# Kernel optimization log

Measured on AMD Instinct MI355X. Metric: run time of the kernel, lower is better.

## Reference

```python
import jax, jax.numpy as jnp
import numpy as np

N_KNN = 16
BN_EPS = 1e-5


def conv1d(x, w, b):
    # x: [B, Cin, N], w: [Cout, Cin], b: [Cout] (1x1 Conv1d)
    return jnp.einsum('oc,bcn->bon', w, x) + b[None, :, None]


def conv2d(x, w, b):
    # x: [B, Cin, N, K], w: [Cout, Cin], b: [Cout] (1x1 Conv2d)
    return jnp.einsum('oc,bcnk->bonk', w, x) + b[None, :, None, None]


def bn2d(x, gamma, beta, mean, var):
    # eval-mode BatchNorm2d over channel axis 1
    scale = (gamma / jnp.sqrt(var + BN_EPS))[None, :, None, None]
    return (x - mean[None, :, None, None]) * scale + beta[None, :, None, None]


def knn_idx(pos, k):
    # pos: [B, 3, N] -> idx: [B, N, K] of k nearest neighbors (incl. self)
    p = jnp.swapaxes(pos, 1, 2)  # [B, N, 3]
    sq = jnp.sum(p * p, axis=-1)  # [B, N]
    d2 = sq[:, :, None] - 2.0 * jnp.einsum('bnd,bmd->bnm', p, p) + sq[:, None, :]
    _, idx = jax.lax.top_k(-d2, k)
    return idx


def group(x, idx):
    # x: [B, C, N], idx: [B, N, K] -> [B, C, N, K] (grouping_operation)
    return jax.vmap(lambda xb, ib: xb[:, ib])(x, idx)


def setup_inputs() -> dict:
    key = jax.random.key(0)
    B, C_OBJ, C_Q, N, DIM, PH, AM = 4, 512, 512, 4096, 128, 64, 4
    ks = jax.random.split(key, 32)
    r = lambda i, sh, s=0.05: jax.random.normal(ks[i], sh, jnp.float32) * s
    inp = {
        'obj_feature': jax.random.normal(ks[0], (B, C_OBJ, N), jnp.float32),
        'pos': jax.random.normal(ks[1], (B, 3, N), jnp.float32),
        'query_points': jax.random.normal(ks[2], (B, C_Q, N), jnp.float32),
        # linear_start_query / linear_start_obj
        'w_sq': r(3, (DIM, C_Q)), 'b_sq': r(4, (DIM,)),
        'w_so': r(5, (DIM, C_OBJ)), 'b_so': r(6, (DIM,)),
        # key / query / value 1x1 convs
        'w_k': r(7, (DIM, DIM)), 'b_k': r(8, (DIM,)),
        'w_q': r(9, (DIM, DIM)), 'b_q': r(10, (DIM,)),
        'w_v': r(11, (DIM, DIM)), 'b_v': r(12, (DIM,)),
        # pos_mlp: Conv2d(3->PH), BN, ReLU, Conv2d(PH->DIM)
        'w_p1': r(13, (PH, 3)), 'b_p1': r(14, (PH,)),
        'g_bn1': 1.0 + r(15, (PH,)), 'be_bn1': r(16, (PH,)),
        'm_bn1': r(17, (PH,)), 'v_bn1': 1.0 + 0.1 * jax.random.uniform(ks[18], (PH,), jnp.float32),
        'w_p2': r(19, (DIM, PH)), 'b_p2': r(20, (DIM,)),
        # attn_mlp: Conv2d(DIM->DIM*AM), BN, ReLU, Conv2d(DIM*AM->DIM)
        'w_a1': r(21, (DIM * AM, DIM)), 'b_a1': r(22, (DIM * AM,)),
        'g_bn2': 1.0 + r(23, (DIM * AM,)), 'be_bn2': r(24, (DIM * AM,)),
        'm_bn2': r(25, (DIM * AM,)), 'v_bn2': 1.0 + 0.1 * jax.random.uniform(ks[26], (DIM * AM,), jnp.float32),
        # linear_end
        'w_e': r(27, (C_OBJ, DIM)), 'b_e': r(28, (C_OBJ,)),
    }
    return inp


def reference(obj_feature, pos, query_points, w_sq, b_sq, w_so, b_so, w_k, b_k,
              w_q, b_q, w_v, b_v, w_p1, b_p1, g_bn1, be_bn1, m_bn1, v_bn1,
              w_p2, b_p2, w_a1, b_a1, g_bn2, be_bn2, m_bn2, v_bn2, w_e, b_e):
    qf = conv1d(query_points, w_sq, b_sq)          # [B, dim, N]
    f = conv1d(obj_feature, w_so, b_so)            # [B, dim, N]
    idx = knn_idx(jax.lax.stop_gradient(pos), N_KNN)  # [B, N, K]
    key_g = group(conv1d(f, w_k, b_k), idx)        # [B, dim, N, K]
    value = conv1d(f, w_v, b_v)                    # [B, dim, N]
    query = conv1d(qf, w_q, b_q)                   # [B, dim, N]
    qk_rel = query[:, :, :, None] - key_g          # [B, dim, N, K]
    pos_rel = pos[:, :, :, None] - group(pos, idx)  # [B, 3, N, K]
    pe = conv2d(jax.nn.relu(bn2d(conv2d(pos_rel, w_p1, b_p1), g_bn1, be_bn1, m_bn1, v_bn1)), w_p2, b_p2)
    attn = conv2d(jax.nn.relu(bn2d(conv2d(qk_rel + pe, w_a1, b_a1), g_bn2, be_bn2, m_bn2, v_bn2)), w_a2_placeholder := w_p2 * 0 + 0, b_p2 * 0) if False else None
    hidden = jax.nn.relu(bn2d(conv2d(qk_rel + pe, w_a1, b_a1), g_bn2, be_bn2, m_bn2, v_bn2))
    attn = jax.nn.softmax(conv2d(hidden, w_a2, b_a2), axis=-1)  # softmax over K
    v = value[:, :, :, None] + pe                  # [B, dim, N, K]
    agg = jnp.sum(attn * v, axis=-1)               # 'b c i j, b c i j -> b c i'
    return conv1d(agg, w_e, b_e)                   # [B, C_obj, N]

# fix: w_a2/b_a2 are parameters; re-declare reference cleanly to include them

def _setup_extra(inp):
    kk = jax.random.split(jax.random.key(7), 2)
    inp['w_a2'] = jax.random.normal(kk[0], (128, 512), jnp.float32) * 0.05
    inp['b_a2'] = jax.random.normal(kk[1], (128,), jnp.float32) * 0.05
    return inp

_orig_setup = setup_inputs

def setup_inputs():
    return _setup_extra(_orig_setup())


def reference(obj_feature, pos, query_points, w_sq, b_sq, w_so, b_so, w_k, b_k,
              w_q, b_q, w_v, b_v, w_p1, b_p1, g_bn1, be_bn1, m_bn1, v_bn1,
              w_p2, b_p2, w_a1, b_a1, g_bn2, be_bn2, m_bn2, v_bn2, w_a2, b_a2,
              w_e, b_e):
    qf = conv1d(query_points, w_sq, b_sq)
    f = conv1d(obj_feature, w_so, b_so)
    idx = knn_idx(jax.lax.stop_gradient(pos), N_KNN)
    key_g = group(conv1d(f, w_k, b_k), idx)
    value = conv1d(f, w_v, b_v)
    query = conv1d(qf, w_q, b_q)
    qk_rel = query[:, :, :, None] - key_g
    pos_rel = pos[:, :, :, None] - group(pos, idx)
    pe = conv2d(jax.nn.relu(bn2d(conv2d(pos_rel, w_p1, b_p1), g_bn1, be_bn1, m_bn1, v_bn1)), w_p2, b_p2)
    hidden = jax.nn.relu(bn2d(conv2d(qk_rel + pe, w_a1, b_a1), g_bn2, be_bn2, m_bn2, v_bn2))
    attn = jax.nn.softmax(conv2d(hidden, w_a2, b_a2), axis=-1)
    v = value[:, :, :, None] + pe
    agg = jnp.sum(attn * v, axis=-1)
    return conv1d(agg, w_e, b_e)
```

## Files before the change

### kernel.cpp

```cpp
#include <hip/hip_runtime.h>

typedef __bf16 bf16;
typedef __bf16 bf16x8 __attribute__((ext_vector_type(8)));
typedef __bf16 bf16x4 __attribute__((ext_vector_type(4)));
typedef __bf16 bf16x2 __attribute__((ext_vector_type(2)));
typedef float f32x4 __attribute__((ext_vector_type(4)));

#define MFMA16(a,b,c) __builtin_amdgcn_mfma_f32_16x16x32_bf16((a),(b),(c),0,0,0)

#define NPTS 4096
#define CIN 512
#define DIM 128
#define PH 64
#define HID 512

#define OFF_WQS 0u
#define OFF_WKO (128u*1024u)
#define OFF_WVO (256u*1024u)
#define OFF_BQS (384u*1024u)
#define OFF_BKO (385u*1024u)
#define OFF_BVO (386u*1024u)
#define OFF_S1  (387u*1024u)
#define OFF_T1  (388u*1024u)
#define OFF_S2  (389u*1024u)
#define OFF_T2  (391u*1024u)
#define OFF_CW  (400u*1024u)
#define OFF_QT  (1u<<20)
#define OFF_KT  (OFF_QT + (4u<<20))
#define OFF_VT  (OFF_QT + (8u<<20))
#define OFF_IDX (OFF_QT + (12u<<20))
#define WS_NEED (OFF_QT + (13u<<20))

struct P {
  const float* in[31];
  char* ws;
  float* out;
  int ybase;
};

__device__ __forceinline__ void softbar() {
  asm volatile("s_waitcnt lgkmcnt(0)" ::: "memory");
  __builtin_amdgcn_s_barrier();
  __builtin_amdgcn_sched_barrier(0);
}

template<int C> __device__ __forceinline__ float rorf(float x){
  return __int_as_float(__builtin_amdgcn_mov_dpp(__float_as_int(x), 0x120|C, 0xF, 0xF, true));
}
__device__ __forceinline__ float red16max(float x){
  x=fmaxf(x,rorf<1>(x)); x=fmaxf(x,rorf<2>(x)); x=fmaxf(x,rorf<4>(x)); x=fmaxf(x,rorf<8>(x)); return x;
}
__device__ __forceinline__ float red16sum(float x){
  x+=rorf<1>(x); x+=rorf<2>(x); x+=rorf<4>(x); x+=rorf<8>(x); return x;
}
template<int C> __device__ __forceinline__ unsigned long long ror64(unsigned long long k){
  unsigned lo = (unsigned)__builtin_amdgcn_mov_dpp((int)(unsigned)k,        0x120|C, 0xF, 0xF, true);
  unsigned hi = (unsigned)__builtin_amdgcn_mov_dpp((int)(unsigned)(k>>32), 0x120|C, 0xF, 0xF, true);
  return ((unsigned long long)hi<<32)|lo;
}

__global__ __launch_bounds__(256) void k_fold(P p) {
  int tid = blockIdx.x*256 + threadIdx.x;
  char* ws = p.ws;
  if (tid < 196608) {
    int m_id = tid >> 16, o = (tid >> 9) & 127, c = tid & 511;
    const float* A  = m_id==0 ? p.in[9] : (m_id==1 ? p.in[7] : p.in[11]);
    const float* Bm = (m_id==0) ? p.in[3] : p.in[5];
    float acc = 0.f;
    #pragma unroll 8
    for (int m=0;m<128;m++) acc += A[o*128+m] * Bm[m*512+c];
    bf16* outw = (bf16*)(ws + (m_id==0?OFF_WQS: m_id==1?OFF_WKO:OFF_WVO));
    outw[o*512+c] = (bf16)acc;
  } else if (tid < 196992) {
    int t = tid - 196608; int m_id = t >> 7, o = t & 127;
    const float* A  = m_id==0 ? p.in[9] : (m_id==1 ? p.in[7] : p.in[11]);
    const float* bb = (m_id==0) ? p.in[4] : p.in[6];
    const float* bs = m_id==0 ? p.in[10] : (m_id==1 ? p.in[8] : p.in[12]);
    float acc = bs[o];
    for (int m=0;m<128;m++) acc += A[o*128+m] * bb[m];
    float* ob = (float*)(ws + (m_id==0?OFF_BQS: m_id==1?OFF_BKO:OFF_BVO));
    ob[o] = acc;
  } else if (tid < 197056) {
    int i = tid - 196992;
    float s = p.in[15][i] * rsqrtf(p.in[18][i] + 1e-5f);
    ((float*)(ws+OFF_S1))[i] = s;
    ((float*)(ws+OFF_T1))[i] = (p.in[14][i] - p.in[17][i])*s + p.in[16][i];
  } else if (tid < 197568) {
    int i = tid - 197056;
    float s = p.in[23][i] * rsqrtf(p.in[26][i] + 1e-5f);
    ((float*)(ws+OFF_S2))[i] = s;
    ((float*)(ws+OFF_T2))[i] = (p.in[22][i] - p.in[25][i])*s + p.in[24][i];
  } else if (tid < 223168) {
    int e0 = (tid - 197568) * 8;
    const float* src; int base;
    if (e0 < 8192)        { src = p.in[19]; base = 0; }
    else if (e0 < 73728)  { src = p.in[21]; base = 8192; }
    else if (e0 < 139264) { src = p.in[29]; base = 73728; }
    else                  { src = p.in[27]; base = 139264; }
    const float* sp = src + (e0 - base);
    f32x4 a = *(const f32x4*)sp, b2 = *(const f32x4*)(sp+4);
    bf16x8 o8;
    o8[0]=(bf16)a[0]; o8[1]=(bf16)a[1]; o8[2]=(bf16)a[2]; o8[3]=(bf16)a[3];
    o8[4]=(bf16)b2[0]; o8[5]=(bf16)b2[1]; o8[6]=(bf16)b2[2]; o8[7]=(bf16)b2[3];
    *(bf16x8*)((bf16*)(ws+OFF_CW) + e0) = o8;
  }
}

__global__ __launch_bounds__(256) void k_knnqkv(P p) {
  if (blockIdx.x < 768) {
    int qb = blockIdx.x;
    int mat = qb >> 8, b = (qb >> 6) & 3, n0 = (qb & 63) * 64;
    int tid = threadIdx.x, lane = tid&63, w = tid>>6;
    const float* in = (mat==0 ? p.in[2] : p.in[0]) + b*CIN*NPTS;
    const bf16* W = (const bf16*)(p.ws + (mat==0?OFF_WQS: mat==1?OFF_WKO:OFF_WVO));
    const float* bias = (const float*)(p.ws + (mat==0?OFF_BQS: mat==1?OFF_BKO:OFF_BVO));
    bf16* outT = (bf16*)(p.ws + (mat==0?OFF_QT: mat==1?OFF_KT:OFF_VT)) + (b*NPTS + n0)*DIM;
    __shared__ __align__(16) bf16 Bl[64*40];
    f32x4 acc[8] = {};
    for (int ks=0; ks<16; ks++) {
      int c0 = ks*32;
      {
        int cc = tid>>3, nn0 = (tid&7)*8;
        const float* sp = in + (c0+cc)*NPTS + n0 + nn0;
        f32x4 a = *(const f32x4*)sp, b2 = *(const f32x4*)(sp+4);
        Bl[(nn0+0)*40+cc]=(bf16)a[0];  Bl[(nn0+1)*40+cc]=(bf16)a[1];
        Bl[(nn0+2)*40+cc]=(bf16)a[2];  Bl[(nn0+3)*40+cc]=(bf16)a[3];
        Bl[(nn0+4)*40+cc]=(bf16)b2[0]; Bl[(nn0+5)*40+cc]=(bf16)b2[1];
        Bl[(nn0+6)*40+cc]=(bf16)b2[2]; Bl[(nn0+7)*40+cc]=(bf16)b2[3];
      }
      softbar();
      int ncol = w*16 + (lane&15);
      bf16x8 bfr = *(const bf16x8*)(&Bl[ncol*40 + (lane>>4)*8]);
      #pragma unroll
      for (int ot=0;ot<8;ot++) {
        bf16x8 af = *(const bf16x8*)(W + (ot*16 + (lane&15))*CIN + c0 + (lane>>4)*8);
        acc[ot] = MFMA16(af, bfr, acc[ot]);
      }
      softbar();
    }
    int o0 = (lane>>4)*4;
    int nloc = w*16 + (lane&15);
    #pragma unroll
    for (int ot=0;ot<8;ot++) {
      f32x4 bs = *(const f32x4*)(bias + ot*16 + o0);
      bf16x4 st;
      st[0]=(bf16)(acc[ot][0]+bs[0]); st[1]=(bf16)(acc[ot][1]+bs[1]);
      st[2]=(bf16)(acc[ot][2]+bs[2]); st[3]=(bf16)(acc[ot][3]+bs[3]);
      *(bf16x4*)(outT + nloc*DIM + ot*16 + o0) = st;
    }
    return;
  }
  int lane = threadIdx.x & 63, w = threadIdx.x >> 6;
  int ig = (blockIdx.x - 768)*4 + w;
  int b = ig >> 12, n = ig & 4095;
  const float* pb = p.in[1] + b*3*NPTS;
  float qx = pb[n], qy = pb[NPTS+n], qz = pb[2*NPTS+n];
  float sqn = __fadd_rn(__fadd_rn(__fmul_rn(qx,qx), __fmul_rn(qy,qy)), __fmul_rn(qz,qz));
  unsigned u[64];
  #pragma unroll
  for (int t=0;t<64;t++) {
    int j = t*64 + lane;
    float xj=pb[j], yj=pb[NPTS+j], zj=pb[2*NPTS+j];
    float sqj = __fadd_rn(__fadd_rn(__fmul_rn(xj,xj), __fmul_rn(yj,yj)), __fmul_rn(zj,zj));
    float dot = __fadd_rn(__fadd_rn(__fmul_rn(qx,xj), __fmul_rn(qy,yj)), __fmul_rn(qz,zj));
    float d2 = __fadd_rn(__fsub_rn(sqn, __fmul_rn(2.f,dot)), sqj);
    unsigned bb2 = __float_as_uint(d2);
    u[t] = bb2 ^ (((unsigned)((int)bb2 >> 31)) | 0x80000000u);
  }
  unsigned v0=u[0], v1=u[16], v2=u[32], v3=u[48];
  int t0=0, t1=16, t2=32, t3=48;
  #pragma unroll
  for (int i=1;i<16;i++) {
    { bool lt=u[i]    <v0; v0=lt?u[i]   :v0; t0=lt?(i)   :t0; }
    { bool lt=u[16+i] <v1; v1=lt?u[16+i]:v1; t1=lt?(16+i):t1; }
    { bool lt=u[32+i] <v2; v2=lt?u[32+i]:v2; t2=lt?(32+i):t2; }
    { bool lt=u[48+i] <v3; v3=lt?u[48+i]:v3; t3=lt?(48+i):t3; }
  }
  int* op = (int*)(p.ws + OFF_IDX) + ig*16;
  #pragma unroll 1
  for (int r=0;r<16;r++) {
    unsigned va=v0; int ta=t0;
    { bool lt=v1<va; va=lt?v1:va; ta=lt?t1:ta; }
    unsigned vb=v2; int tb=t2;
    { bool lt=v3<vb; vb=lt?v3:vb; tb=lt?t3:tb; }
    { bool lt=vb<va; va=lt?vb:va; ta=lt?tb:ta; }
    unsigned long long key = ((unsigned long long)va << 12) | (unsigned)((ta<<6) | lane);
    { unsigned long long o = ror64<1>(key); if (o<key) key=o; }
    { unsigned long long o = ror64<2>(key); if (o<key) key=o; }
    { unsigned long long o = ror64<4>(key); if (o<key) key=o; }
    { unsigned long long o = ror64<8>(key); if (o<key) key=o; }
    { unsigned long long o = __shfl_xor(key,16); if (o<key) key=o; }
    { unsigned long long o = __shfl_xor(key,32); if (o<key) key=o; }
    unsigned jwin = (unsigned)key & 4095u;
    if (lane==0) op[r] = (int)jwin;
    if (r==15) break;
    int tsel = __builtin_amdgcn_readfirstlane((int)(jwin>>6));
    bool mine = ((int)(jwin&63)==lane);
    switch (tsel) {
#define CLR(T) case T: u[T] = mine ? 0xFFFFFFFFu : u[T]; break;
      CLR(0) CLR(1) CLR(2) CLR(3) CLR(4) CLR(5) CLR(6) CLR(7)
      CLR(8) CLR(9) CLR(10) CLR(11) CLR(12) CLR(13) CLR(14) CLR(15)
      CLR(16) CLR(17) CLR(18) CLR(19) CLR(20) CLR(21) CLR(22) CLR(23)
      CLR(24) CLR(25) CLR(26) CLR(27) CLR(28) CLR(29) CLR(30) CLR(31)
      CLR(32) CLR(33) CLR(34) CLR(35) CLR(36) CLR(37) CLR(38) CLR(39)
      CLR(40) CLR(41) CLR(42) CLR(43) CLR(44) CLR(45) CLR(46) CLR(47)
      CLR(48) CLR(49) CLR(50) CLR(51) CLR(52) CLR(53) CLR(54) CLR(55)
      CLR(56) CLR(57) CLR(58) CLR(59) CLR(60) CLR(61) CLR(62) CLR(63)
#undef CLR
      default: break;
    }
    switch (tsel >> 4) {
      case 0: { v0=u[0]; t0=0;
        #pragma unroll
        for (int i=1;i<16;i++){ bool lt=u[i]<v0; v0=lt?u[i]:v0; t0=lt?i:t0; } } break;
      case 1: { v1=u[16]; t1=16;
        #pragma unroll
        for (int i=1;i<16;i++){ bool lt=u[16+i]<v1; v1=lt?u[16+i]:v1; t1=lt?(16+i):t1; } } break;
      case 2: { v2=u[32]; t2=32;
        #pragma unroll
        for (int i=1;i<16;i++){ bool lt=u[32+i]<v2; v2=lt?u[32+i]:v2; t2=lt?(32+i):t2; } } break;
      default: { v3=u[48]; t3=48;
        #pragma unroll
        for (int i=1;i<16;i++){ bool lt=u[48+i]<v3; v3=lt?u[48+i]:v3; t3=lt?(48+i):t3; } } break;
    }
  }
}

__global__ __launch_bounds__(512) void k_fused(P p) {
  int bb = p.ybase + blockIdx.y, pt0 = blockIdx.x*8;
  int tid=threadIdx.x, lane=tid&63, w=tid>>6;
  int c = lane&15, g = lane>>4;
  char* ws = p.ws;
  const bf16* qT = (const bf16*)(ws+OFF_QT) + bb*NPTS*DIM;
  const bf16* kT = (const bf16*)(ws+OFF_KT) + bb*NPTS*DIM;
  const bf16* vT = (const bf16*)(ws+OFF_VT) + bb*NPTS*DIM;
  const int* idxg = (const int*)(ws+OFF_IDX) + (bb*NPTS + pt0)*16;
  const bf16* wp2b = (const bf16*)(ws+OFF_CW);
  const bf16* wa1b = wp2b + 8192;
  const bf16* wa2b = wa1b + 65536;
  const bf16* web  = wa2b + 65536;
  const float* s2 = (const float*)(ws+OFF_S2);
  const float* t2 = (const float*)(ws+OFF_T2);
  __shared__ __align__(16) char LB[53248];
  bf16* Xl = (bf16*)LB;
  bf16* HT = (bf16*)(LB + 34816);
  bf16* aggl = (bf16*)(LB + 34816);

  {
    int col = w*16 + c;
    int j = idxg[col] & 4095;
    const float* pb = p.in[1] + bb*3*NPTS;
    int n = pt0 + w;
    float r0 = pb[n]-pb[j], r1 = pb[NPTS+n]-pb[NPTS+j], r2 = pb[2*NPTS+n]-pb[2*NPTS+j];
    const float* wp1 = p.in[13];
    const float* s1 = (const float*)(ws+OFF_S1);
    const float* t1 = (const float*)(ws+OFF_T1);
    #pragma unroll
    for (int i=0;i<16;i+=2) {
      int m = g*16 + i;
      float x0 = wp1[m*3]*r0   + wp1[m*3+1]*r1 + wp1[m*3+2]*r2;
      float x1 = wp1[m*3+3]*r0 + wp1[m*3+4]*r1 + wp1[m*3+5]*r2;
      bf16x2 pk;
      pk[0] = (bf16)fmaxf(0.f, x0*s1[m]   + t1[m]);
      pk[1] = (bf16)fmaxf(0.f, x1*s1[m+1] + t1[m+1]);
      *(bf16x2*)(&HT[col*72 + m]) = pk;
    }
  }
  softbar();

  {
    f32x4 acc[8] = {};
    int crow = w*16 + c;
    #pragma unroll
    for (int ksx=0; ksx<2; ksx++) {
      int m0 = ksx*32 + g*8;
      bf16x8 af = *(const bf16x8*)(wp2b + crow*PH + m0);
      #pragma unroll
      for (int nt=0; nt<8; nt++) {
        int col = nt*16 + c;
        bf16x8 bfr = *(const bf16x8*)(&HT[col*72 + m0]);
        acc[nt] = MFMA16(af, bfr, acc[nt]);
      }
    }
    int c0 = w*16 + g*4;
    f32x4 bp4 = *(const f32x4*)(p.in[20] + c0);
    #pragma unroll
    for (int nt=0; nt<8; nt++) {
      int col = nt*16 + c;
      int j = idxg[col] & 4095;
      int n = pt0 + nt;
      bf16x4 q4 = *(const bf16x4*)(qT + n*DIM + c0);
      bf16x4 k4 = *(const bf16x4*)(kT + j*DIM + c0);
      bf16x4 st;
      #pragma unroll
      for (int r=0;r<4;r++)
        st[r] = (bf16)((float)q4[r] - (float)k4[r] + acc[nt][r] + bp4[r]);
      *(bf16x4*)(&Xl[col*136 + c0]) = st;
    }
  }
  softbar();

  f32x4 S[8] = {};
  for (int ch=0; ch<8; ch++) {
    f32x4 acc1[4] = {};
    int mtw = w & 3, nbase = (w>>2)*4;
    int hrow = ch*64 + mtw*16 + c;
    #pragma unroll
    for (int ksx=0; ksx<4; ksx++) {
      bf16x8 af = *(const bf16x8*)(wa1b + hrow*DIM + ksx*32 + g*8);
      #pragma unroll
      for (int i=0; i<4; i++) {
        int col = (nbase+i)*16 + c;
        bf16x8 bfr = *(const bf16x8*)(&Xl[col*136 + ksx*32 + g*8]);
        acc1[i] = MFMA16(af, bfr, acc1[i]);
      }
    }
    int h0 = ch*64 + mtw*16 + g*4;
    int h0loc = mtw*16 + g*4;
    f32x4 sv = *(const f32x4*)(s2 + h0);
    f32x4 tv = *(const f32x4*)(t2 + h0);
    #pragma unroll
    for (int i=0;i<4;i++) {
      int col = (nbase+i)*16 + c;
      bf16x4 st;
      st[0]=(bf16)fmaxf(0.f, acc1[i][0]*sv[0]+tv[0]);
      st[1]=(bf16)fmaxf(0.f, acc1[i][1]*sv[1]+tv[1]);
      st[2]=(bf16)fmaxf(0.f, acc1[i][2]*sv[2]+tv[2]);
      st[3]=(bf16)fmaxf(0.f, acc1[i][3]*sv[3]+tv[3]);
      *(bf16x4*)(&HT[col*72 + h0loc]) = st;
    }
    softbar();
    int orow = w*16 + c;
    #pragma unroll
    for (int ksx=0; ksx<2; ksx++) {
      bf16x8 af = *(const bf16x8*)(wa2b + orow*HID + ch*64 + ksx*32 + g*8);
      #pragma unroll
      for (int nt=0; nt<8; nt++) {
        int col = nt*16 + c;
        bf16x8 bfr = *(const bf16x8*)(&HT[col*72 + ksx*32 + g*8]);
        S[nt] = MFMA16(af, bfr, S[nt]);
      }
    }
    softbar();
  }

  {
    int c0 = w*16 + g*4;
    #pragma unroll
    for (int nt=0; nt<8; nt++) {
      f32x4 s = S[nt];
      int col = nt*16 + c;
      int j = idxg[col] & 4095;
      int n = pt0 + nt;
      bf16x4 x4 = *(const bf16x4*)(&Xl[col*136 + c0]);
      bf16x4 q4 = *(const bf16x4*)(qT + n*DIM + c0);
      bf16x4 k4 = *(const bf16x4*)(kT + j*DIM + c0);
      bf16x4 v4 = *(const bf16x4*)(vT + n*DIM + c0);
      float agv[4];
      #pragma unroll
      for (int r=0;r<4;r++) {
        float mx = red16max(s[r]);
        float e = __expf(s[r]-mx);
        float sm = red16sum(e);
        float at = e/sm;
        float vpe = (float)v4[r] + (float)x4[r] - (float)q4[r] + (float)k4[r];
        agv[r] = red16sum(at*vpe);
      }
      if (c==0) {
        bf16x4 st; st[0]=(bf16)agv[0]; st[1]=(bf16)agv[1]; st[2]=(bf16)agv[2]; st[3]=(bf16)agv[3];
        *(bf16x4*)(&aggl[nt*136 + c0]) = st;
      }
    }
  }
  softbar();

  {
    const float* be = p.in[28];
    f32x4 acc5[4] = {};
    #pragma unroll
    for (int ksx=0; ksx<4; ksx++) {
      bf16x8 bfr = *(const bf16x8*)(&aggl[c*136 + ksx*32 + g*8]);
      #pragma unroll
      for (int i=0;i<4;i++) {
        int e = (w*4+i)*16 + c;
        bf16x8 af = *(const bf16x8*)(web + e*DIM + ksx*32 + g*8);
        acc5[i] = MFMA16(af, bfr, acc5[i]);
      }
    }
    if (c < 8) {
      int n = pt0 + c;
      #pragma unroll
      for (int i=0;i<4;i++) {
        int e0 = (w*4+i)*16 + g*4;
        f32x4 be4 = *(const f32x4*)(be + e0);
        #pragma unroll
        for (int r=0;r<4;r++)
          p.out[(bb*CIN + e0+r)*NPTS + n] = acc5[i][r] + be4[r];
      }
    }
  }
}

extern "C" void kernel_launch(void* const* d_in, const int* in_sizes, int n_in,
                              void* d_out, int out_size, void* d_ws, size_t ws_size,
                              hipStream_t stream) {
  if (ws_size < WS_NEED || n_in < 31) return;
  P p;
  for (int i=0;i<31;i++) p.in[i] = (const float*)d_in[i];
  p.ws = (char*)d_ws;
  p.out = (float*)d_out;
  p.ybase = 0;
  k_fold<<<872, 256, 0, stream>>>(p);
  k_knnqkv<<<768 + 4096, 256, 0, stream>>>(p);
  k_fused<<<dim3(512, 4), 512, 0, stream>>>(p);
}
```

Before: 400.5 us.

## XOR-swizzle LDS tiles instead of padding and prefetch gathered key rows

Replaces the padded LDS layouts (row strides of 136 and 72 elements) for the X and hidden tiles with unpadded power-of-two rows and an XOR swizzle on the column index. This avoids bank conflicts while shrinking shared memory from 53248 to 49152 bytes. It also loads the kNN indices and gathered key vectors into registers once at kernel start, so they are not re-gathered from global memory in two phases. The trade-off is more live registers (the k4p and jn arrays) across the main loop, which may raise register pressure.

```diff
diff --git a/kernel.cpp b/kernel.cpp
--- a/kernel.cpp
+++ b/kernel.cpp
@@ -226,6 +226,9 @@
   }
 }
 
+#define XLB(LBp, col, off2) ((bf16*)((LBp) + (((((col)<<8) + ((off2)<<1))) ^ ((((col)&7))<<4))))
+#define HTB(LBp, col, off2) ((bf16*)((LBp) + 32768 + (((((col)<<7) + ((off2)<<1))) ^ ((((col)&7))<<4))))
+
 __global__ __launch_bounds__(512) void k_fused(P p) {
   int bb = p.ybase + blockIdx.y, pt0 = blockIdx.x*8;
   int tid=threadIdx.x, lane=tid&63, w=tid>>6;
@@ -241,14 +244,20 @@
   const bf16* web  = wa2b + 65536;
   const float* s2 = (const float*)(ws+OFF_S2);
   const float* t2 = (const float*)(ws+OFF_T2);
-  __shared__ __align__(16) char LB[53248];
-  bf16* Xl = (bf16*)LB;
-  bf16* HT = (bf16*)(LB + 34816);
-  bf16* aggl = (bf16*)(LB + 34816);
+  __shared__ __align__(16) char LB[49152];
+  bf16* aggl = (bf16*)(LB + 32768);
+
+  int c0 = w*16 + g*4;
+  int jn[8];
+  #pragma unroll
+  for (int nt=0;nt<8;nt++) jn[nt] = idxg[nt*16 + c] & 4095;
+  bf16x4 k4p[8];
+  #pragma unroll
+  for (int nt=0;nt<8;nt++) k4p[nt] = *(const bf16x4*)(kT + jn[nt]*DIM + c0);
 
   {
     int col = w*16 + c;
-    int j = idxg[col] & 4095;
+    int j = jn[w];
     const float* pb = p.in[1] + bb*3*NPTS;
     int n = pt0 + w;
     float r0 = pb[n]-pb[j], r1 = pb[NPTS+n]-pb[NPTS+j], r2 = pb[2*NPTS+n]-pb[2*NPTS+j];
@@ -263,7 +272,7 @@
       bf16x2 pk;
       pk[0] = (bf16)fmaxf(0.f, x0*s1[m]   + t1[m]);
       pk[1] = (bf16)fmaxf(0.f, x1*s1[m+1] + t1[m+1]);
-      *(bf16x2*)(&HT[col*72 + m]) = pk;
+      *(bf16x2*)HTB(LB, col, m) = pk;
     }
   }
   softbar();
@@ -278,24 +287,22 @@
       #pragma unroll
       for (int nt=0; nt<8; nt++) {
         int col = nt*16 + c;
-        bf16x8 bfr = *(const bf16x8*)(&HT[col*72 + m0]);
+        bf16x8 bfr = *(const bf16x8*)HTB(LB, col, m0);
         acc[nt] = MFMA16(af, bfr, acc[nt]);
       }
     }
-    int c0 = w*16 + g*4;
     f32x4 bp4 = *(const f32x4*)(p.in[20] + c0);
     #pragma unroll
     for (int nt=0; nt<8; nt++) {
       int col = nt*16 + c;
-      int j = idxg[col] & 4095;
       int n = pt0 + nt;
       bf16x4 q4 = *(const bf16x4*)(qT + n*DIM + c0);
-      bf16x4 k4 = *(const bf16x4*)(kT + j*DIM + c0);
+      bf16x4 k4 = k4p[nt];
       bf16x4 st;
       #pragma unroll
       for (int r=0;r<4;r++)
         st[r] = (bf16)((float)q4[r] - (float)k4[r] + acc[nt][r] + bp4[r]);
-      *(bf16x4*)(&Xl[col*136 + c0]) = st;
+      *(bf16x4*)XLB(LB, col, c0) = st;
     }
   }
   softbar();
@@ -311,7 +318,7 @@
       #pragma unroll
       for (int i=0; i<4; i++) {
         int col = (nbase+i)*16 + c;
-        bf16x8 bfr = *(const bf16x8*)(&Xl[col*136 + ksx*32 + g*8]);
+        bf16x8 bfr = *(const bf16x8*)XLB(LB, col, ksx*32 + g*8);
         acc1[i] = MFMA16(af, bfr, acc1[i]);
       }
     }
@@ -327,7 +334,7 @@
       st[1]=(bf16)fmaxf(0.f, acc1[i][1]*sv[1]+tv[1]);
       st[2]=(bf16)fmaxf(0.f, acc1[i][2]*sv[2]+tv[2]);
       st[3]=(bf16)fmaxf(0.f, acc1[i][3]*sv[3]+tv[3]);
-      *(bf16x4*)(&HT[col*72 + h0loc]) = st;
+      *(bf16x4*)HTB(LB, col, h0loc) = st;
     }
     softbar();
     int orow = w*16 + c;
@@ -337,7 +344,7 @@
       #pragma unroll
       for (int nt=0; nt<8; nt++) {
         int col = nt*16 + c;
-        bf16x8 bfr = *(const bf16x8*)(&HT[col*72 + ksx*32 + g*8]);
+        bf16x8 bfr = *(const bf16x8*)HTB(LB, col, ksx*32 + g*8);
         S[nt] = MFMA16(af, bfr, S[nt]);
       }
     }
@@ -345,16 +352,14 @@
   }
 
   {
-    int c0 = w*16 + g*4;
     #pragma unroll
     for (int nt=0; nt<8; nt++) {
       f32x4 s = S[nt];
       int col = nt*16 + c;
-      int j = idxg[col] & 4095;
       int n = pt0 + nt;
-      bf16x4 x4 = *(const bf16x4*)(&Xl[col*136 + c0]);
+      bf16x4 x4 = *(const bf16x4*)XLB(LB, col, c0);
       bf16x4 q4 = *(const bf16x4*)(qT + n*DIM + c0);
-      bf16x4 k4 = *(const bf16x4*)(kT + j*DIM + c0);
+      bf16x4 k4 = k4p[nt];
       bf16x4 v4 = *(const bf16x4*)(vT + n*DIM + c0);
       float agv[4];
       #pragma unroll
```

Result: slower. 455.1 us (+13.6%).

## Fuse KNN selection into main fused kernel, keep indices in LDS

Applied to the files above, without the earlier changes.

Moves the per-point KNN distance computation and top-16 selection out of the combined qkv/knn kernel into the start of the fused attention kernel. Each of the 8 waves computes neighbours for one point and writes them to shared memory, so the global index buffer write/read round trip goes away. The qkv kernel now launches only the projection blocks. The trade-off is that the fused kernel, launched with 512 threads per block, takes on a register-heavy 64-entry selection phase, which can raise register pressure and cut occupancy for the whole kernel. It also loses the overlap the separate KNN blocks had with the projection GEMM blocks.

```diff
diff --git a/kernel.cpp b/kernel.cpp
--- a/kernel.cpp
+++ b/kernel.cpp
@@ -106,123 +106,46 @@
   }
 }
 
-__global__ __launch_bounds__(256) void k_knnqkv(P p) {
-  if (blockIdx.x < 768) {
-    int qb = blockIdx.x;
-    int mat = qb >> 8, b = (qb >> 6) & 3, n0 = (qb & 63) * 64;
-    int tid = threadIdx.x, lane = tid&63, w = tid>>6;
-    const float* in = (mat==0 ? p.in[2] : p.in[0]) + b*CIN*NPTS;
-    const bf16* W = (const bf16*)(p.ws + (mat==0?OFF_WQS: mat==1?OFF_WKO:OFF_WVO));
-    const float* bias = (const float*)(p.ws + (mat==0?OFF_BQS: mat==1?OFF_BKO:OFF_BVO));
-    bf16* outT = (bf16*)(p.ws + (mat==0?OFF_QT: mat==1?OFF_KT:OFF_VT)) + (b*NPTS + n0)*DIM;
-    __shared__ __align__(16) bf16 Bl[64*40];
-    f32x4 acc[8] = {};
-    for (int ks=0; ks<16; ks++) {
-      int c0 = ks*32;
-      {
-        int cc = tid>>3, nn0 = (tid&7)*8;
-        const float* sp = in + (c0+cc)*NPTS + n0 + nn0;
-        f32x4 a = *(const f32x4*)sp, b2 = *(const f32x4*)(sp+4);
-        Bl[(nn0+0)*40+cc]=(bf16)a[0];  Bl[(nn0+1)*40+cc]=(bf16)a[1];
-        Bl[(nn0+2)*40+cc]=(bf16)a[2];  Bl[(nn0+3)*40+cc]=(bf16)a[3];
-        Bl[(nn0+4)*40+cc]=(bf16)b2[0]; Bl[(nn0+5)*40+cc]=(bf16)b2[1];
-        Bl[(nn0+6)*40+cc]=(bf16)b2[2]; Bl[(nn0+7)*40+cc]=(bf16)b2[3];
-      }
-      softbar();
-      int ncol = w*16 + (lane&15);
-      bf16x8 bfr = *(const bf16x8*)(&Bl[ncol*40 + (lane>>4)*8]);
-      #pragma unroll
-      for (int ot=0;ot<8;ot++) {
-        bf16x8 af = *(const bf16x8*)(W + (ot*16 + (lane&15))*CIN + c0 + (lane>>4)*8);
-        acc[ot] = MFMA16(af, bfr, acc[ot]);
-      }
-      softbar();
-    }
-    int o0 = (lane>>4)*4;
-    int nloc = w*16 + (lane&15);
+__global__ __launch_bounds__(256) void k_qkv(P p) {
+  int qb = blockIdx.x;
+  int mat = qb >> 8, b = (qb >> 6) & 3, n0 = (qb & 63) * 64;
+  int tid = threadIdx.x, lane = tid&63, w = tid>>6;
+  const float* in = (mat==0 ? p.in[2] : p.in[0]) + b*CIN*NPTS;
+  const bf16* W = (const bf16*)(p.ws + (mat==0?OFF_WQS: mat==1?OFF_WKO:OFF_WVO));
+  const float* bias = (const float*)(p.ws + (mat==0?OFF_BQS: mat==1?OFF_BKO:OFF_BVO));
+  bf16* outT = (bf16*)(p.ws + (mat==0?OFF_QT: mat==1?OFF_KT:OFF_VT)) + (b*NPTS + n0)*DIM;
+  __shared__ __align__(16) bf16 Bl[64*40];
+  f32x4 acc[8] = {};
+  for (int ks=0; ks<16; ks++) {
+    int c0 = ks*32;
+    {
+      int cc = tid>>3, nn0 = (tid&7)*8;
+      const float* sp = in + (c0+cc)*NPTS + n0 + nn0;
+      f32x4 a = *(const f32x4*)sp, b2 = *(const f32x4*)(sp+4);
+      Bl[(nn0+0)*40+cc]=(bf16)a[0];  Bl[(nn0+1)*40+cc]=(bf16)a[1];
+      Bl[(nn0+2)*40+cc]=(bf16)a[2];  Bl[(nn0+3)*40+cc]=(bf16)a[3];
+      Bl[(nn0+4)*40+cc]=(bf16)b2[0]; Bl[(nn0+5)*40+cc]=(bf16)b2[1];
+      Bl[(nn0+6)*40+cc]=(bf16)b2[2]; Bl[(nn0+7)*40+cc]=(bf16)b2[3];
+    }
+    softbar();
+    int ncol = w*16 + (lane&15);
+    bf16x8 bfr = *(const bf16x8*)(&Bl[ncol*40 + (lane>>4)*8]);
     #pragma unroll
     for (int ot=0;ot<8;ot++) {
-      f32x4 bs = *(const f32x4*)(bias + ot*16 + o0);
-      bf16x4 st;
-      st[0]=(bf16)(acc[ot][0]+bs[0]); st[1]=(bf16)(acc[ot][1]+bs[1]);
-      st[2]=(bf16)(acc[ot][2]+bs[2]); st[3]=(bf16)(acc[ot][3]+bs[3]);
-      *(bf16x4*)(outT + nloc*DIM + ot*16 + o0) = st;
-    }
-    return;
-  }
-  int lane = threadIdx.x & 63, w = threadIdx.x >> 6;
-  int ig = (blockIdx.x - 768)*4 + w;
-  int b = ig >> 12, n = ig & 4095;
-  const float* pb = p.in[1] + b*3*NPTS;
-  float qx = pb[n], qy = pb[NPTS+n], qz = pb[2*NPTS+n];
-  float sqn = __fadd_rn(__fadd_rn(__fmul_rn(qx,qx), __fmul_rn(qy,qy)), __fmul_rn(qz,qz));
-  unsigned u[64];
+      bf16x8 af = *(const bf16x8*)(W + (ot*16 + (lane&15))*CIN + c0 + (lane>>4)*8);
+      acc[ot] = MFMA16(af, bfr, acc[ot]);
+    }
+    softbar();
+  }
+  int o0 = (lane>>4)*4;
+  int nloc = w*16 + (lane&15);
   #pragma unroll
-  for (int t=0;t<64;t++) {
-    int j = t*64 + lane;
-    float xj=pb[j], yj=pb[NPTS+j], zj=pb[2*NPTS+j];
-    float sqj = __fadd_rn(__fadd_rn(__fmul_rn(xj,xj), __fmul_rn(yj,yj)), __fmul_rn(zj,zj));
-    float dot = __fadd_rn(__fadd_rn(__fmul_rn(qx,xj), __fmul_rn(qy,yj)), __fmul_rn(qz,zj));
-    float d2 = __fadd_rn(__fsub_rn(sqn, __fmul_rn(2.f,dot)), sqj);
-    unsigned bb2 = __float_as_uint(d2);
-    u[t] = bb2 ^ (((unsigned)((int)bb2 >> 31)) | 0x80000000u);
-  }
-  unsigned v0=u[0], v1=u[16], v2=u[32], v3=u[48];
-  int t0=0, t1=16, t2=32, t3=48;
-  #pragma unroll
-  for (int i=1;i<16;i++) {
-    { bool lt=u[i]    <v0; v0=lt?u[i]   :v0; t0=lt?(i)   :t0; }
-    { bool lt=u[16+i] <v1; v1=lt?u[16+i]:v1; t1=lt?(16+i):t1; }
-    { bool lt=u[32+i] <v2; v2=lt?u[32+i]:v2; t2=lt?(32+i):t2; }
-    { bool lt=u[48+i] <v3; v3=lt?u[48+i]:v3; t3=lt?(48+i):t3; }
-  }
-  int* op = (int*)(p.ws + OFF_IDX) + ig*16;
-  #pragma unroll 1
-  for (int r=0;r<16;r++) {
-    unsigned va=v0; int ta=t0;
-    { bool lt=v1<va; va=lt?v1:va; ta=lt?t1:ta; }
-    unsigned vb=v2; int tb=t2;
-    { bool lt=v3<vb; vb=lt?v3:vb; tb=lt?t3:tb; }
-    { bool lt=vb<va; va=lt?vb:va; ta=lt?tb:ta; }
-    unsigned long long key = ((unsigned long long)va << 12) | (unsigned)((ta<<6) | lane);
-    { unsigned long long o = ror64<1>(key); if (o<key) key=o; }
-    { unsigned long long o = ror64<2>(key); if (o<key) key=o; }
-    { unsigned long long o = ror64<4>(key); if (o<key) key=o; }
-    { unsigned long long o = ror64<8>(key); if (o<key) key=o; }
-    { unsigned long long o = __shfl_xor(key,16); if (o<key) key=o; }
-    { unsigned long long o = __shfl_xor(key,32); if (o<key) key=o; }
-    unsigned jwin = (unsigned)key & 4095u;
-    if (lane==0) op[r] = (int)jwin;
-    if (r==15) break;
-    int tsel = __builtin_amdgcn_readfirstlane((int)(jwin>>6));
-    bool mine = ((int)(jwin&63)==lane);
-    switch (tsel) {
-#define CLR(T) case T: u[T] = mine ? 0xFFFFFFFFu : u[T]; break;
-      CLR(0) CLR(1) CLR(2) CLR(3) CLR(4) CLR(5) CLR(6) CLR(7)
-      CLR(8) CLR(9) CLR(10) CLR(11) CLR(12) CLR(13) CLR(14) CLR(15)
-      CLR(16) CLR(17) CLR(18) CLR(19) CLR(20) CLR(21) CLR(22) CLR(23)
-      CLR(24) CLR(25) CLR(26) CLR(27) CLR(28) CLR(29) CLR(30) CLR(31)
-      CLR(32) CLR(33) CLR(34) CLR(35) CLR(36) CLR(37) CLR(38) CLR(39)
-      CLR(40) CLR(41) CLR(42) CLR(43) CLR(44) CLR(45) CLR(46) CLR(47)
-      CLR(48) CLR(49) CLR(50) CLR(51) CLR(52) CLR(53) CLR(54) CLR(55)
-      CLR(56) CLR(57) CLR(58) CLR(59) CLR(60) CLR(61) CLR(62) CLR(63)
-#undef CLR
-      default: break;
-    }
-    switch (tsel >> 4) {
-      case 0: { v0=u[0]; t0=0;
-        #pragma unroll
-        for (int i=1;i<16;i++){ bool lt=u[i]<v0; v0=lt?u[i]:v0; t0=lt?i:t0; } } break;
-      case 1: { v1=u[16]; t1=16;
-        #pragma unroll
-        for (int i=1;i<16;i++){ bool lt=u[16+i]<v1; v1=lt?u[16+i]:v1; t1=lt?(16+i):t1; } } break;
-      case 2: { v2=u[32]; t2=32;
-        #pragma unroll
-        for (int i=1;i<16;i++){ bool lt=u[32+i]<v2; v2=lt?u[32+i]:v2; t2=lt?(32+i):t2; } } break;
-      default: { v3=u[48]; t3=48;
-        #pragma unroll
-        for (int i=1;i<16;i++){ bool lt=u[48+i]<v3; v3=lt?u[48+i]:v3; t3=lt?(48+i):t3; } } break;
-    }
+  for (int ot=0;ot<8;ot++) {
+    f32x4 bs = *(const f32x4*)(bias + ot*16 + o0);
+    bf16x4 st;
+    st[0]=(bf16)(acc[ot][0]+bs[0]); st[1]=(bf16)(acc[ot][1]+bs[1]);
+    st[2]=(bf16)(acc[ot][2]+bs[2]); st[3]=(bf16)(acc[ot][3]+bs[3]);
+    *(bf16x4*)(outT + nloc*DIM + ot*16 + o0) = st;
   }
 }
 
@@ -234,7 +157,6 @@
   const bf16* qT = (const bf16*)(ws+OFF_QT) + bb*NPTS*DIM;
   const bf16* kT = (const bf16*)(ws+OFF_KT) + bb*NPTS*DIM;
   const bf16* vT = (const bf16*)(ws+OFF_VT) + bb*NPTS*DIM;
-  const int* idxg = (const int*)(ws+OFF_IDX) + (bb*NPTS + pt0)*16;
   const bf16* wp2b = (const bf16*)(ws+OFF_CW);
   const bf16* wa1b = wp2b + 8192;
   const bf16* wa2b = wa1b + 65536;
@@ -245,11 +167,87 @@
   bf16* Xl = (bf16*)LB;
   bf16* HT = (bf16*)(LB + 34816);
   bf16* aggl = (bf16*)(LB + 34816);
+  __shared__ int idxl[128];
+
+  const float* pb = p.in[1] + bb*3*NPTS;
+
+  {
+    int n = pt0 + w;
+    float qx = pb[n], qy = pb[NPTS+n], qz = pb[2*NPTS+n];
+    float sqn = __fadd_rn(__fadd_rn(__fmul_rn(qx,qx), __fmul_rn(qy,qy)), __fmul_rn(qz,qz));
+    unsigned u[64];
+    #pragma unroll
+    for (int t=0;t<64;t++) {
+      int j = t*64 + lane;
+      float xj=pb[j], yj=pb[NPTS+j], zj=pb[2*NPTS+j];
+      float sqj = __fadd_rn(__fadd_rn(__fmul_rn(xj,xj), __fmul_rn(yj,yj)), __fmul_rn(zj,zj));
+      float dot = __fadd_rn(__fadd_rn(__fmul_rn(qx,xj), __fmul_rn(qy,yj)), __fmul_rn(qz,zj));
+      float d2 = __fadd_rn(__fsub_rn(sqn, __fmul_rn(2.f,dot)), sqj);
+      unsigned bb2 = __float_as_uint(d2);
+      u[t] = bb2 ^ (((unsigned)((int)bb2 >> 31)) | 0x80000000u);
+    }
+    unsigned v0=u[0], v1=u[16], v2=u[32], v3=u[48];
+    int t0=0, t1=16, t2_=32, t3=48;
+    #pragma unroll
+    for (int i=1;i<16;i++) {
+      { bool lt=u[i]    <v0; v0=lt?u[i]   :v0; t0=lt?(i)   :t0; }
+      { bool lt=u[16+i] <v1; v1=lt?u[16+i]:v1; t1=lt?(16+i):t1; }
+      { bool lt=u[32+i] <v2; v2=lt?u[32+i]:v2; t2_=lt?(32+i):t2_; }
+      { bool lt=u[48+i] <v3; v3=lt?u[48+i]:v3; t3=lt?(48+i):t3; }
+    }
+    #pragma unroll 1
+    for (int r=0;r<16;r++) {
+      unsigned va=v0; int ta=t0;
+      { bool lt=v1<va; va=lt?v1:va; ta=lt?t1:ta; }
+      unsigned vb=v2; int tb=t2_;
+      { bool lt=v3<vb; vb=lt?v3:vb; tb=lt?t3:tb; }
+      { bool lt=vb<va; va=lt?vb:va; ta=lt?tb:ta; }
+      unsigned long long key = ((unsigned long long)va << 12) | (unsigned)((ta<<6) | lane);
+      { unsigned long long o = ror64<1>(key); if (o<key) key=o; }
+      { unsigned long long o = ror64<2>(key); if (o<key) key=o; }
+      { unsigned long long o = ror64<4>(key); if (o<key) key=o; }
+      { unsigned long long o = ror64<8>(key); if (o<key) key=o; }
+      { unsigned long long o = __shfl_xor(key,16); if (o<key) key=o; }
+      { unsigned long long o = __shfl_xor(key,32); if (o<key) key=o; }
+      unsigned jwin = (unsigned)key & 4095u;
+      if (lane==0) idxl[w*16 + r] = (int)jwin;
+      if (r==15) break;
+      int tsel = __builtin_amdgcn_readfirstlane((int)(jwin>>6));
+      bool mine = ((int)(jwin&63)==lane);
+      switch (tsel) {
+#define CLR(T) case T: u[T] = mine ? 0xFFFFFFFFu : u[T]; break;
+        CLR(0) CLR(1) CLR(2) CLR(3) CLR(4) CLR(5) CLR(6) CLR(7)
+        CLR(8) CLR(9) CLR(10) CLR(11) CLR(12) CLR(13) CLR(14) CLR(15)
+        CLR(16) CLR(17) CLR(18) CLR(19) CLR(20) CLR(21) CLR(22) CLR(23)
+        CLR(24) CLR(25) CLR(26) CLR(27) CLR(28) CLR(29) CLR(30) CLR(31)
+        CLR(32) CLR(33) CLR(34) CLR(35) CLR(36) CLR(37) CLR(38) CLR(39)
+        CLR(40) CLR(41) CLR(42) CLR(43) CLR(44) CLR(45) CLR(46) CLR(47)
+        CLR(48) CLR(49) CLR(50) CLR(51) CLR(52) CLR(53) CLR(54) CLR(55)
+        CLR(56) CLR(57) CLR(58) CLR(59) CLR(60) CLR(61) CLR(62) CLR(63)
+#undef CLR
+        default: break;
+      }
+      switch (tsel >> 4) {
+        case 0: { v0=u[0]; t0=0;
+          #pragma unroll
+          for (int i=1;i<16;i++){ bool lt=u[i]<v0; v0=lt?u[i]:v0; t0=lt?i:t0; } } break;
+        case 1: { v1=u[16]; t1=16;
+          #pragma unroll
+          for (int i=1;i<16;i++){ bool lt=u[16+i]<v1; v1=lt?u[16+i]:v1; t1=lt?(16+i):t1; } } break;
+        case 2: { v2=u[32]; t2_=32;
+          #pragma unroll
+          for (int i=1;i<16;i++){ bool lt=u[32+i]<v2; v2=lt?u[32+i]:v2; t2_=lt?(32+i):t2_; } } break;
+        default: { v3=u[48]; t3=48;
+          #pragma unroll
+          for (int i=1;i<16;i++){ bool lt=u[48+i]<v3; v3=lt?u[48+i]:v3; t3=lt?(48+i):t3; } } break;
+      }
+    }
+  }
+  softbar();
 
   {
     int col = w*16 + c;
-    int j = idxg[col] & 4095;
-    const float* pb = p.in[1] + bb*3*NPTS;
+    int j = idxl[col];
     int n = pt0 + w;
     float r0 = pb[n]-pb[j], r1 = pb[NPTS+n]-pb[NPTS+j], r2 = pb[2*NPTS+n]-pb[2*NPTS+j];
     const float* wp1 = p.in[13];
@@ -287,7 +285,7 @@
     #pragma unroll
     for (int nt=0; nt<8; nt++) {
       int col = nt*16 + c;
-      int j = idxg[col] & 4095;
+      int j = idxl[col];
       int n = pt0 + nt;
       bf16x4 q4 = *(const bf16x4*)(qT + n*DIM + c0);
       bf16x4 k4 = *(const bf16x4*)(kT + j*DIM + c0);
@@ -350,7 +348,7 @@
     for (int nt=0; nt<8; nt++) {
       f32x4 s = S[nt];
       int col = nt*16 + c;
-      int j = idxg[col] & 4095;
+      int j = idxl[col];
       int n = pt0 + nt;
       bf16x4 x4 = *(const bf16x4*)(&Xl[col*136 + c0]);
       bf16x4 q4 = *(const bf16x4*)(qT + n*DIM + c0);
@@ -411,6 +409,6 @@
   p.out = (float*)d_out;
   p.ybase = 0;
   k_fold<<<872, 256, 0, stream>>>(p);
-  k_knnqkv<<<768 + 4096, 256, 0, stream>>>(p);
+  k_qkv<<<768, 256, 0, stream>>>(p);
   k_fused<<<dim3(512, 4), 512, 0, stream>>>(p);
 }
```

Result: slower. 466.9 us (+16.6%).

## Split KNN top-k search across four waves per query with shared-memory merge

Applied to the files above, without the earlier changes.

The KNN selection now assigns one block of four waves to each query point instead of one wave per point. Each wave holds 16 candidate distances per lane rather than 64 and publishes its running minimum to shared memory, where the four slots are merged each round. Only the wave owning the winner rescans its candidates. This aims to reduce register pressure and raise occupancy and parallelism, at the cost of block barriers per extraction round and idle waves during the rescan.

```diff
diff --git a/kernel.cpp b/kernel.cpp
--- a/kernel.cpp
+++ b/kernel.cpp
@@ -107,10 +107,10 @@
 }
 
 __global__ __launch_bounds__(256) void k_knnqkv(P p) {
+  int tid = threadIdx.x, lane = tid&63, w = tid>>6;
   if (blockIdx.x < 768) {
     int qb = blockIdx.x;
     int mat = qb >> 8, b = (qb >> 6) & 3, n0 = (qb & 63) * 64;
-    int tid = threadIdx.x, lane = tid&63, w = tid>>6;
     const float* in = (mat==0 ? p.in[2] : p.in[0]) + b*CIN*NPTS;
     const bf16* W = (const bf16*)(p.ws + (mat==0?OFF_WQS: mat==1?OFF_WKO:OFF_WVO));
     const float* bias = (const float*)(p.ws + (mat==0?OFF_BQS: mat==1?OFF_BKO:OFF_BVO));
@@ -150,79 +150,71 @@
     }
     return;
   }
-  int lane = threadIdx.x & 63, w = threadIdx.x >> 6;
-  int ig = (blockIdx.x - 768)*4 + w;
-  int b = ig >> 12, n = ig & 4095;
+  __shared__ unsigned long long slot[4];
+  int pt = blockIdx.x - 768;
+  int b = pt >> 12, n = pt & 4095;
   const float* pb = p.in[1] + b*3*NPTS;
   float qx = pb[n], qy = pb[NPTS+n], qz = pb[2*NPTS+n];
   float sqn = __fadd_rn(__fadd_rn(__fmul_rn(qx,qx), __fmul_rn(qy,qy)), __fmul_rn(qz,qz));
-  unsigned u[64];
+  unsigned u[16];
   #pragma unroll
-  for (int t=0;t<64;t++) {
-    int j = t*64 + lane;
+  for (int i=0;i<16;i++) {
+    int j = w*1024 + i*64 + lane;
     float xj=pb[j], yj=pb[NPTS+j], zj=pb[2*NPTS+j];
     float sqj = __fadd_rn(__fadd_rn(__fmul_rn(xj,xj), __fmul_rn(yj,yj)), __fmul_rn(zj,zj));
     float dot = __fadd_rn(__fadd_rn(__fmul_rn(qx,xj), __fmul_rn(qy,yj)), __fmul_rn(qz,zj));
     float d2 = __fadd_rn(__fsub_rn(sqn, __fmul_rn(2.f,dot)), sqj);
     unsigned bb2 = __float_as_uint(d2);
-    u[t] = bb2 ^ (((unsigned)((int)bb2 >> 31)) | 0x80000000u);
-  }
-  unsigned v0=u[0], v1=u[16], v2=u[32], v3=u[48];
-  int t0=0, t1=16, t2=32, t3=48;
-  #pragma unroll
-  for (int i=1;i<16;i++) {
-    { bool lt=u[i]    <v0; v0=lt?u[i]   :v0; t0=lt?(i)   :t0; }
-    { bool lt=u[16+i] <v1; v1=lt?u[16+i]:v1; t1=lt?(16+i):t1; }
-    { bool lt=u[32+i] <v2; v2=lt?u[32+i]:v2; t2=lt?(32+i):t2; }
-    { bool lt=u[48+i] <v3; v3=lt?u[48+i]:v3; t3=lt?(48+i):t3; }
-  }
-  int* op = (int*)(p.ws + OFF_IDX) + ig*16;
-  #pragma unroll 1
-  for (int r=0;r<16;r++) {
-    unsigned va=v0; int ta=t0;
-    { bool lt=v1<va; va=lt?v1:va; ta=lt?t1:ta; }
-    unsigned vb=v2; int tb=t2;
-    { bool lt=v3<vb; vb=lt?v3:vb; tb=lt?t3:tb; }
-    { bool lt=vb<va; va=lt?vb:va; ta=lt?tb:ta; }
-    unsigned long long key = ((unsigned long long)va << 12) | (unsigned)((ta<<6) | lane);
+    u[i] = bb2 ^ (((unsigned)((int)bb2 >> 31)) | 0x80000000u);
+  }
+  {
+    unsigned v = u[0]; int ti = 0;
+    #pragma unroll
+    for (int i=1;i<16;i++) { bool lt = u[i]<v; v = lt?u[i]:v; ti = lt?i:ti; }
+    unsigned long long key = ((unsigned long long)v << 12) | (unsigned)(w*1024 + ti*64 + lane);
     { unsigned long long o = ror64<1>(key); if (o<key) key=o; }
     { unsigned long long o = ror64<2>(key); if (o<key) key=o; }
     { unsigned long long o = ror64<4>(key); if (o<key) key=o; }
     { unsigned long long o = ror64<8>(key); if (o<key) key=o; }
     { unsigned long long o = __shfl_xor(key,16); if (o<key) key=o; }
     { unsigned long long o = __shfl_xor(key,32); if (o<key) key=o; }
-    unsigned jwin = (unsigned)key & 4095u;
-    if (lane==0) op[r] = (int)jwin;
+    if (lane==0) slot[w] = key;
+  }
+  __syncthreads();
+  int* op = (int*)(p.ws + OFF_IDX) + pt*16;
+  #pragma unroll 1
+  for (int r=0;r<16;r++) {
+    unsigned long long k0=slot[0], k1=slot[1], k2=slot[2], k3=slot[3];
+    unsigned long long ka = (k1<k0)?k1:k0;
+    unsigned long long kb = (k3<k2)?k3:k2;
+    unsigned long long bk = (kb<ka)?kb:ka;
+    unsigned jwin = (unsigned)bk & 4095u;
+    if (tid==0) op[r] = (int)jwin;
     if (r==15) break;
-    int tsel = __builtin_amdgcn_readfirstlane((int)(jwin>>6));
-    bool mine = ((int)(jwin&63)==lane);
-    switch (tsel) {
+    __syncthreads();
+    if (w == (int)(jwin>>10)) {
+      int isel = (int)((jwin>>6)&15);
+      bool mine = ((int)(jwin&63) == lane);
+      switch (isel) {
 #define CLR(T) case T: u[T] = mine ? 0xFFFFFFFFu : u[T]; break;
-      CLR(0) CLR(1) CLR(2) CLR(3) CLR(4) CLR(5) CLR(6) CLR(7)
-      CLR(8) CLR(9) CLR(10) CLR(11) CLR(12) CLR(13) CLR(14) CLR(15)
-      CLR(16) CLR(17) CLR(18) CLR(19) CLR(20) CLR(21) CLR(22) CLR(23)
-      CLR(24) CLR(25) CLR(26) CLR(27) CLR(28) CLR(29) CLR(30) CLR(31)
-      CLR(32) CLR(33) CLR(34) CLR(35) CLR(36) CLR(37) CLR(38) CLR(39)
-      CLR(40) CLR(41) CLR(42) CLR(43) CLR(44) CLR(45) CLR(46) CLR(47)
-      CLR(48) CLR(49) CLR(50) CLR(51) CLR(52) CLR(53) CLR(54) CLR(55)
-      CLR(56) CLR(57) CLR(58) CLR(59) CLR(60) CLR(61) CLR(62) CLR(63)
+        CLR(0) CLR(1) CLR(2) CLR(3) CLR(4) CLR(5) CLR(6) CLR(7)
+        CLR(8) CLR(9) CLR(10) CLR(11) CLR(12) CLR(13) CLR(14) CLR(15)
 #undef CLR
-      default: break;
-    }
-    switch (tsel >> 4) {
-      case 0: { v0=u[0]; t0=0;
-        #pragma unroll
-        for (int i=1;i<16;i++){ bool lt=u[i]<v0; v0=lt?u[i]:v0; t0=lt?i:t0; } } break;
-      case 1: { v1=u[16]; t1=16;
-        #pragma unroll
-        for (int i=1;i<16;i++){ bool lt=u[16+i]<v1; v1=lt?u[16+i]:v1; t1=lt?(16+i):t1; } } break;
-      case 2: { v2=u[32]; t2=32;
-        #pragma unroll
-        for (int i=1;i<16;i++){ bool lt=u[32+i]<v2; v2=lt?u[32+i]:v2; t2=lt?(32+i):t2; } } break;
-      default: { v3=u[48]; t3=48;
-        #pragma unroll
-        for (int i=1;i<16;i++){ bool lt=u[48+i]<v3; v3=lt?u[48+i]:v3; t3=lt?(48+i):t3; } } break;
-    }
+        default: break;
+      }
+      unsigned v = u[0]; int ti = 0;
+      #pragma unroll
+      for (int i=1;i<16;i++) { bool lt = u[i]<v; v = lt?u[i]:v; ti = lt?i:ti; }
+      unsigned long long key = ((unsigned long long)v << 12) | (unsigned)(w*1024 + ti*64 + lane);
+      { unsigned long long o = ror64<1>(key); if (o<key) key=o; }
+      { unsigned long long o = ror64<2>(key); if (o<key) key=o; }
+      { unsigned long long o = ror64<4>(key); if (o<key) key=o; }
+      { unsigned long long o = ror64<8>(key); if (o<key) key=o; }
+      { unsigned long long o = __shfl_xor(key,16); if (o<key) key=o; }
+      { unsigned long long o = __shfl_xor(key,32); if (o<key) key=o; }
+      if (lane==0) slot[w] = key;
+    }
+    __syncthreads();
   }
 }
 
@@ -411,6 +403,6 @@
   p.out = (float*)d_out;
   p.ybase = 0;
   k_fold<<<872, 256, 0, stream>>>(p);
-  k_knnqkv<<<768 + 4096, 256, 0, stream>>>(p);
+  k_knnqkv<<<768 + 16384, 256, 0, stream>>>(p);
   k_fused<<<dim3(512, 4), 512, 0, stream>>>(p);
 }
```

Result: slower. 429.8 us (+7.3%).
